# Performance work log

Hardware: AMD Instinct MI355X
Metric: run time of the kernel (lower is better)

The kernel has to match this reference:

```python
import jax, jax.numpy as jnp
from jax import lax
import numpy as np

DN = ('NDHWC', 'DHWIO', 'NDHWC')

def conv3d(x, w, b, stride=1):
    return lax.conv_general_dilated(x, w, (stride,) * 3, 'SAME', dimension_numbers=DN) + b

def convT3d(x, w, b, stride=2):
    return lax.conv_transpose(x, w, (stride,) * 3, 'SAME', dimension_numbers=DN) + b

def prelu(x, a):
    return jnp.where(x > 0, x, a * x)

def bn(x, g, be, m, v):
    # keras BatchNormalization, inference mode, epsilon=1e-3
    return (x - m) * g * lax.rsqrt(v + 1e-3) + be

def res_unit(x, c1w, c1b, c2w, c2b, g, be, m, v, a):
    # VQVAEResidualUnit: relu(x + PReLU(BN(conv2(swish(conv1(x))))))
    h = jax.nn.swish(conv3d(x, c1w, c1b))
    h = prelu(bn(conv3d(h, c2w, c2b), g, be, m, v), a)
    return jax.nn.relu(x + h)

def _forward(x, ec0_w, ec0_b, er0_c1w, er0_c1b, er0_c2w, er0_c2b, er0_g, er0_be, er0_m, er0_v, er0_a, ec1_w, ec1_b, er1_c1w, er1_c1b, er1_c2w, er1_c2b, er1_g, er1_be, er1_m, er1_v, er1_a, eo_w, eo_b, eo_a, codebook, dc0_w, dc0_b, dc0_a, dr0_c1w, dr0_c1b, dr0_c2w, dr0_c2b, dr0_g, dr0_be, dr0_m, dr0_v, dr0_a, du0_w, du0_b, dr1_c1w, dr1_c1b, dr1_c2w, dr1_c2b, dr1_g, dr1_be, dr1_m, dr1_v, dr1_a, du1_w, du1_b):
    # ----- Encoder -----
    h = jax.nn.relu(conv3d(x, ec0_w, ec0_b, stride=2))   # [B,64,64,64,64]
    h = res_unit(h, er0_c1w, er0_c1b, er0_c2w, er0_c2b, er0_g, er0_be, er0_m, er0_v, er0_a)
    h = jax.nn.relu(conv3d(h, ec1_w, ec1_b, stride=2))   # [B,32,32,32,128]
    h = res_unit(h, er1_c1w, er1_c1b, er1_c2w, er1_c2b, er1_g, er1_be, er1_m, er1_v, er1_a)
    z = prelu(conv3d(h, eo_w, eo_b), eo_a)               # [B,32,32,32,64] latent
    # ----- NSVQ (inference: hard codebook lookup) -----
    D = z.shape[-1]
    flat = z.reshape(-1, D)                              # [N, 64], N = B*32^3
    dist = (flat * flat).sum(1, keepdims=True) + (codebook * codebook).sum(1) - 2.0 * (flat @ codebook.T)  # [N, K]
    idx = jnp.argmin(dist, axis=1)
    zq = codebook[idx].reshape(z.shape)
    K = codebook.shape[0]
    p = jnp.zeros((K,), jnp.float32).at[idx].add(1.0) / flat.shape[0]
    perplexity = jnp.exp(-jnp.sum(p * jnp.log(p + 1e-12)))
    # ----- Decoder -----
    h = prelu(conv3d(zq, dc0_w, dc0_b), dc0_a)           # [B,32,32,32,128]
    h = res_unit(h, dr0_c1w, dr0_c1b, dr0_c2w, dr0_c2b, dr0_g, dr0_be, dr0_m, dr0_v, dr0_a)
    h = jax.nn.relu(convT3d(h, du0_w, du0_b))            # [B,64,64,64,64]
    h = res_unit(h, dr1_c1w, dr1_c1b, dr1_c2w, dr1_c2b, dr1_g, dr1_be, dr1_m, dr1_v, dr1_a)
    recon = convT3d(h, du1_w, du1_b)                     # [B,128,128,128,1]
    return recon, perplexity

def setup_inputs() -> dict:
    key = jax.random.key(0)
    ks = iter(jax.random.split(key, 40))
    nrm = lambda *s: jax.random.normal(next(ks), s, jnp.float32) * 0.05
    def ru(pfx, c):
        return {pfx + '_c1w': nrm(3, 3, 3, c, c), pfx + '_c1b': jnp.zeros((c,), jnp.float32),
                pfx + '_c2w': nrm(3, 3, 3, c, c), pfx + '_c2b': jnp.zeros((c,), jnp.float32),
                pfx + '_g': jnp.ones((c,), jnp.float32), pfx + '_be': jnp.zeros((c,), jnp.float32),
                pfx + '_m': jnp.zeros((c,), jnp.float32), pfx + '_v': jnp.ones((c,), jnp.float32),
                pfx + '_a': jnp.full((c,), 0.25, jnp.float32)}
    C0, C1, D, K = 64, 128, 64, 512
    inp = {'x': jax.random.normal(next(ks), (2, 128, 128, 128, 1), jnp.float32)}
    inp.update(ec0_w=nrm(4, 4, 4, 1, C0), ec0_b=jnp.zeros((C0,), jnp.float32))
    inp.update(ru('er0', C0))
    inp.update(ec1_w=nrm(4, 4, 4, C0, C1), ec1_b=jnp.zeros((C1,), jnp.float32))
    inp.update(ru('er1', C1))
    inp.update(eo_w=nrm(3, 3, 3, C1, D), eo_b=jnp.zeros((D,), jnp.float32), eo_a=jnp.full((D,), 0.25, jnp.float32))
    inp.update(codebook=jax.random.uniform(next(ks), (K, D), jnp.float32, -1.0, 1.0) * np.sqrt(6.0 / D).astype(np.float32))
    inp.update(dc0_w=nrm(3, 3, 3, D, C1), dc0_b=jnp.zeros((C1,), jnp.float32), dc0_a=jnp.full((C1,), 0.25, jnp.float32))
    inp.update(ru('dr0', C1))
    inp.update(du0_w=nrm(4, 4, 4, C1, C0), du0_b=jnp.zeros((C0,), jnp.float32))
    inp.update(ru('dr1', C0))
    inp.update(du1_w=nrm(4, 4, 4, C0, 1), du1_b=jnp.zeros((1,), jnp.float32))
    return inp

def reference(x, ec0_w, ec0_b, er0_c1w, er0_c1b, er0_c2w, er0_c2b, er0_g, er0_be, er0_m, er0_v, er0_a, ec1_w, ec1_b, er1_c1w, er1_c1b, er1_c2w, er1_c2b, er1_g, er1_be, er1_m, er1_v, er1_a, eo_w, eo_b, eo_a, codebook, dc0_w, dc0_b, dc0_a, dr0_c1w, dr0_c1b, dr0_c2w, dr0_c2b, dr0_g, dr0_be, dr0_m, dr0_v, dr0_a, du0_w, du0_b, dr1_c1w, dr1_c1b, dr1_c2w, dr1_c2b, dr1_g, dr1_be, dr1_m, dr1_v, dr1_a, du1_w, du1_b):
    return _forward(x, ec0_w, ec0_b, er0_c1w, er0_c1b, er0_c2w, er0_c2b, er0_g, er0_be, er0_m, er0_v, er0_a, ec1_w, ec1_b, er1_c1w, er1_c1b, er1_c2w, er1_c2b, er1_g, er1_be, er1_m, er1_v, er1_a, eo_w, eo_b, eo_a, codebook, dc0_w, dc0_b, dc0_a, dr0_c1w, dr0_c1b, dr0_c2w, dr0_c2b, dr0_g, dr0_be, dr0_m, dr0_v, dr0_a, du0_w, du0_b, dr1_c1w, dr1_c1b, dr1_c2w, dr1_c2b, dr1_g, dr1_be, dr1_m, dr1_v, dr1_a, du1_w, du1_b)
```

## Files before the change

kernel.cpp:

```cpp
#include <hip/hip_runtime.h>
#include <cstdint>


typedef unsigned short bf16_t;
typedef __attribute__((ext_vector_type(8)))  short s8b;
typedef __attribute__((ext_vector_type(16))) float f32x16;

__device__ __forceinline__ float b2f(bf16_t u) { return __uint_as_float((unsigned)u << 16); }
__device__ __forceinline__ bf16_t f2b(float f) {
    unsigned x = __float_as_uint(f);
    return (bf16_t)((x + 0x7FFFu + ((x >> 16) & 1u)) >> 16);
}

__device__ __forceinline__ void split3s(float v, unsigned short& h,
                                        unsigned short& m, unsigned short& l)
{
    const unsigned uv = __float_as_uint(v);
    const float fh = __uint_as_float(uv & 0xFFFF0000u);
    const float r1 = v - fh;
    const unsigned u1 = __float_as_uint(r1);
    const float fm = __uint_as_float(u1 & 0xFFFF0000u);
    const float r2 = r1 - fm;
    h = (unsigned short)(uv >> 16);
    m = (unsigned short)(u1 >> 16);
    l = (unsigned short)(__float_as_uint(r2) >> 16);
}

__device__ __forceinline__ int wdst(int tap, int ci_, int co_, int ci, int co)
{
    const int ks = ci_ >> 4, half = (ci_ >> 3) & 1, j = ci_ & 7;
    return (((tap * (ci >> 4) + ks) * 2 + half) * co + co_) * 8 + j;
}

__global__ __launch_bounds__(256)
void wprep3(const float* __restrict__ w, bf16_t* __restrict__ h,
            bf16_t* __restrict__ m, bf16_t* __restrict__ l,
            int ci, int co, int n)
{
    const int i = blockIdx.x * 256 + threadIdx.x;
    if (i >= n) return;
    const int co_ = i % co;
    const int ci_ = (i / co) % ci;
    const int tap = i / (co * ci);
    const int dst = wdst(tap, ci_, co_, ci, co);
    unsigned short hh, mm, ll2;
    split3s(w[i], hh, mm, ll2);
    h[dst] = hh; m[dst] = mm; l[dst] = ll2;
}

__global__ __launch_bounds__(256)
void wprep_split(const float* __restrict__ w, bf16_t* __restrict__ hi,
                 bf16_t* __restrict__ lo, int ci, int co, int n)
{
    const int i = blockIdx.x * 256 + threadIdx.x;
    if (i >= n) return;
    const int co_ = i % co;
    const int ci_ = (i / co) % ci;
    const int tap = i / (co * ci);
    const float v = w[i];
    const int dst = wdst(tap, ci_, co_, ci, co);
    const bf16_t h = f2b(v);
    hi[dst] = h;
    lo[dst] = f2b(v - b2f(h));
}

template<int CIN, int COUT, int SD, int NWC, int EPI>
__global__ __launch_bounds__((SD / 32) * NWC * 64)
void conv3e(const float* __restrict__ xf,
            const bf16_t* __restrict__ wh, const bf16_t* __restrict__ wm,
            const bf16_t* __restrict__ wl,
            const float* __restrict__ bias,
            const float* __restrict__ g, const float* __restrict__ be,
            const float* __restrict__ mn, const float* __restrict__ vr,
            const float* __restrict__ al,
            const float* skf, float* __restrict__ of)
{
    constexpr int NT   = (SD / 32) * NWC * 64;
    constexpr int LP   = (SD * CIN) / (4 * NT);
    constexpr int KS   = CIN / 16;
    constexpr int ROWS = SD + 2;
    constexpr int RB   = ROWS * CIN;
    __shared__ bf16_t lh[2][RB], lm[2][RB], ll[2][RB];

    const int tid  = threadIdx.x;
    const int lane = tid & 63;
    const int wid  = tid >> 6;
    const int wn   = wid % NWC, wm2 = wid / NWC;
    const int half = lane >> 5, ln = lane & 31;
    const int w    = wm2 * 32 + ln;
    const int nwg  = gridDim.x;
    const int bid  = (blockIdx.x & 7) * (nwg >> 3) + (blockIdx.x >> 3);
    const int h    = bid % SD;
    const int d    = (bid / SD) % SD;
    const int b    = bid / (SD * SD);
    const int cout = wn * 32 + ln;

    int pz[9], py[9], pt[9], np = 0;
    for (int kd = 0; kd < 3; ++kd) {
        const int iz = d + kd - 1;
        if ((unsigned)iz >= (unsigned)SD) continue;
        for (int kh = 0; kh < 3; ++kh) {
            const int iy = h + kh - 1;
            if ((unsigned)iy >= (unsigned)SD) continue;
            pz[np] = iz; py[np] = iy; pt[np] = (kd * 3 + kh) * 3; ++np;
        }
    }

    f32x16 accA, accB;
#pragma unroll
    for (int i = 0; i < 16; ++i) { accA[i] = 0.f; accB[i] = 0.f; }

    for (int i = tid; i < CIN; i += NT) {
        const int bf2 = i / (CIN / 2);
        const int r   = i % (CIN / 2);
        const int gg  = r >> 2;
        const int row = ((r >> 1) & 1) ? (SD + 1) : 0;
        const int so  = (gg * ROWS + row) * 8 + (r & 1) * 4;
        const ushort4 z4 = make_ushort4(0, 0, 0, 0);
        *reinterpret_cast<ushort4*>(&lh[bf2][so]) = z4;
        *reinterpret_cast<ushort4*>(&lm[bf2][so]) = z4;
        *reinterpret_cast<ushort4*>(&ll[bf2][so]) = z4;
    }

    float4 rg[LP];
    auto loadrow = [&](int iz, int iy) {
        const float* src = xf + ((size_t)((b * SD + iz) * SD + iy)) * SD * CIN;
#pragma unroll
        for (int j = 0; j < LP; ++j)
            rg[j] = *reinterpret_cast<const float4*>(src + (size_t)(tid + j * NT) * 4);
    };
    auto writerow = [&](int bf2) {
#pragma unroll
        for (int j = 0; j < LP; ++j) {
            const int idx = (tid + j * NT) * 4;
            const int pv = idx / CIN + 1, ch = idx % CIN;
            ushort4 h4, m4, l4;
            split3s(rg[j].x, h4.x, m4.x, l4.x);
            split3s(rg[j].y, h4.y, m4.y, l4.y);
            split3s(rg[j].z, h4.z, m4.z, l4.z);
            split3s(rg[j].w, h4.w, m4.w, l4.w);
            const int so = ((ch >> 3) * ROWS + pv) * 8 + (ch & 7);
            *reinterpret_cast<ushort4*>(&lh[bf2][so]) = h4;
            *reinterpret_cast<ushort4*>(&lm[bf2][so]) = m4;
            *reinterpret_cast<ushort4*>(&ll[bf2][so]) = l4;
        }
    };

    loadrow(pz[0], py[0]);
    writerow(0);
    if (np > 1) loadrow(pz[1], py[1]);
    __syncthreads();
#pragma unroll 1
    for (int i = 0; i < np; ++i) {
        const int cur = i & 1;
        if (i + 1 < np) writerow((i + 1) & 1);
        if (i + 2 < np) loadrow(pz[i + 2], py[i + 2]);
#pragma unroll
        for (int kw = 0; kw < 3; ++kw) {
            const int tap = pt[i] + kw;
            const int pv = w + kw;
#pragma unroll
            for (int ks = 0; ks < KS; ++ks) {
                const int so = ((ks * 2 + half) * ROWS + pv) * 8;
                const s8b ah  = *reinterpret_cast<const s8b*>(&lh[cur][so]);
                const s8b am  = *reinterpret_cast<const s8b*>(&lm[cur][so]);
                const s8b al3 = *reinterpret_cast<const s8b*>(&ll[cur][so]);
                const size_t wb = ((size_t)((tap * KS + ks) * 2 + half) * COUT + cout) * 8;
                const s8b bh = *reinterpret_cast<const s8b*>(wh + wb);
                const s8b bm = *reinterpret_cast<const s8b*>(wm + wb);
                const s8b bl = *reinterpret_cast<const s8b*>(wl + wb);
                accA = __builtin_amdgcn_mfma_f32_32x32x16_bf16(ah, bh, accA, 0, 0, 0);
                accB = __builtin_amdgcn_mfma_f32_32x32x16_bf16(ah, bm, accB, 0, 0, 0);
                accA = __builtin_amdgcn_mfma_f32_32x32x16_bf16(am, bh, accA, 0, 0, 0);
                accB = __builtin_amdgcn_mfma_f32_32x32x16_bf16(am, bm, accB, 0, 0, 0);
                accA = __builtin_amdgcn_mfma_f32_32x32x16_bf16(al3, bh, accA, 0, 0, 0);
                accB = __builtin_amdgcn_mfma_f32_32x32x16_bf16(ah, bl, accB, 0, 0, 0);
            }
        }
        __syncthreads();
    }

    const size_t outrow = ((size_t)((b * SD + d) * SD + h)) * SD;
    const float bv = bias[cout];
    float sc = 0.f, mm = 0.f, bb2 = 0.f, aa = 0.f;
    if constexpr (EPI == 3) {
        sc = g[cout] * (1.0f / sqrtf(vr[cout] + 1e-3f));
        mm = mn[cout]; bb2 = be[cout]; aa = al[cout];
    }
    if constexpr (EPI == 2) aa = al[cout];
#pragma unroll
    for (int r = 0; r < 16; ++r) {
        const int rl = (r & 3) + 8 * (r >> 2) + 4 * half;
        const size_t oe = (outrow + wm2 * 32 + rl) * COUT + cout;
        float y = accA[r] + accB[r] + bv;
        if constexpr (EPI == 0) y = fmaxf(y, 0.f);
        else if constexpr (EPI == 1) y = y / (1.f + expf(-y));
        else if constexpr (EPI == 2) y = y > 0.f ? y : aa * y;
        else {
            float t2 = (y - mm) * sc + bb2;
            t2 = t2 > 0.f ? t2 : aa * t2;
            y = fmaxf(skf[oe] + t2, 0.f);
        }
        of[oe] = y;
    }
}

__global__ __launch_bounds__(256)
void convs2e(const float* __restrict__ xf,
             const bf16_t* __restrict__ wh, const bf16_t* __restrict__ wm,
             const bf16_t* __restrict__ wl,
             const float* __restrict__ bias, float* __restrict__ of)
{
    constexpr int NT = 256, LP = (64 * 64) / (4 * NT);
    constexpr int ROWS = 66;
    __shared__ bf16_t lh[2][66 * 64], lm[2][66 * 64], ll[2][66 * 64];

    const int tid  = threadIdx.x;
    const int lane = tid & 63;
    const int wn   = tid >> 6;
    const int half = lane >> 5, ln = lane & 31;
    const int nwg  = gridDim.x;
    const int bid  = (blockIdx.x & 7) * (nwg >> 3) + (blockIdx.x >> 3);
    const int h    = bid % 32;
    const int d    = (bid / 32) % 32;
    const int b    = bid / 1024;
    const int cout = wn * 32 + ln;

    int pz[16], py[16], pt[16], np = 0;
    for (int kd = 0; kd < 4; ++kd) {
        const int iz = 2 * d + kd - 1;
        if ((unsigned)iz >= 64u) continue;
        for (int kh = 0; kh < 4; ++kh) {
            const int iy = 2 * h + kh - 1;
            if ((unsigned)iy >= 64u) continue;
            pz[np] = iz; py[np] = iy; pt[np] = (kd * 4 + kh) * 4; ++np;
        }
    }

    f32x16 accA, accB;
#pragma unroll
    for (int i = 0; i < 16; ++i) { accA[i] = 0.f; accB[i] = 0.f; }

    for (int i = tid; i < 64; i += NT) {
        const int bf2 = i / 32;
        const int r   = i % 32;
        const int gg  = r >> 2;
        const int row = ((r >> 1) & 1) ? 65 : 0;
        const int so  = (gg * ROWS + row) * 8 + (r & 1) * 4;
        const ushort4 z4 = make_ushort4(0, 0, 0, 0);
        *reinterpret_cast<ushort4*>(&lh[bf2][so]) = z4;
        *reinterpret_cast<ushort4*>(&lm[bf2][so]) = z4;
        *reinterpret_cast<ushort4*>(&ll[bf2][so]) = z4;
    }

    float4 rg[LP];
    auto loadrow = [&](int iz, int iy) {
        const float* src = xf + ((size_t)((b * 64 + iz) * 64 + iy)) * 64 * 64;
#pragma unroll
        for (int j = 0; j < LP; ++j)
            rg[j] = *reinterpret_cast<const float4*>(src + (size_t)(tid + j * NT) * 4);
    };
    auto writerow = [&](int bf2) {
#pragma unroll
        for (int j = 0; j < LP; ++j) {
            const int idx = (tid + j * NT) * 4;
            const int pv = idx / 64 + 1, ch = idx % 64;
            ushort4 h4, m4, l4;
            split3s(rg[j].x, h4.x, m4.x, l4.x);
            split3s(rg[j].y, h4.y, m4.y, l4.y);
            split3s(rg[j].z, h4.z, m4.z, l4.z);
            split3s(rg[j].w, h4.w, m4.w, l4.w);
            const int so = ((ch >> 3) * ROWS + pv) * 8 + (ch & 7);
            *reinterpret_cast<ushort4*>(&lh[bf2][so]) = h4;
            *reinterpret_cast<ushort4*>(&lm[bf2][so]) = m4;
            *reinterpret_cast<ushort4*>(&ll[bf2][so]) = l4;
        }
    };

    loadrow(pz[0], py[0]);
    writerow(0);
    if (np > 1) loadrow(pz[1], py[1]);
    __syncthreads();
#pragma unroll 1
    for (int i = 0; i < np; ++i) {
        const int cur = i & 1;
        if (i + 1 < np) writerow((i + 1) & 1);
        if (i + 2 < np) loadrow(pz[i + 2], py[i + 2]);
#pragma unroll
        for (int kw = 0; kw < 4; ++kw) {
            const int tap = pt[i] + kw;
            const int pv = 2 * ln + kw;
#pragma unroll
            for (int ks = 0; ks < 4; ++ks) {
                const int so = ((ks * 2 + half) * ROWS + pv) * 8;
                const s8b ah  = *reinterpret_cast<const s8b*>(&lh[cur][so]);
                const s8b am  = *reinterpret_cast<const s8b*>(&lm[cur][so]);
                const s8b al3 = *reinterpret_cast<const s8b*>(&ll[cur][so]);
                const size_t wb = ((size_t)((tap * 4 + ks) * 2 + half) * 128 + cout) * 8;
                const s8b bh = *reinterpret_cast<const s8b*>(wh + wb);
                const s8b bm = *reinterpret_cast<const s8b*>(wm + wb);
                const s8b bl = *reinterpret_cast<const s8b*>(wl + wb);
                accA = __builtin_amdgcn_mfma_f32_32x32x16_bf16(ah, bh, accA, 0, 0, 0);
                accB = __builtin_amdgcn_mfma_f32_32x32x16_bf16(ah, bm, accB, 0, 0, 0);
                accA = __builtin_amdgcn_mfma_f32_32x32x16_bf16(am, bh, accA, 0, 0, 0);
                accB = __builtin_amdgcn_mfma_f32_32x32x16_bf16(am, bm, accB, 0, 0, 0);
                accA = __builtin_amdgcn_mfma_f32_32x32x16_bf16(al3, bh, accA, 0, 0, 0);
                accB = __builtin_amdgcn_mfma_f32_32x32x16_bf16(ah, bl, accB, 0, 0, 0);
            }
        }
        __syncthreads();
    }

    const size_t outrow = ((size_t)((b * 32 + d) * 32 + h)) * 32;
    const float bv = bias[cout];
#pragma unroll
    for (int r = 0; r < 16; ++r) {
        const int rl = (r & 3) + 8 * (r >> 2) + 4 * half;
        const size_t oe = (outrow + rl) * 128 + cout;
        of[oe] = fmaxf(accA[r] + accB[r] + bv, 0.f);
    }
}

template<int CIN, int COUT, int SD, int NWC, int EPI>
__global__ __launch_bounds__((SD / 32) * NWC * 64)
void conv3d(const bf16_t* __restrict__ xh, const bf16_t* __restrict__ xl,
            const bf16_t* __restrict__ wh, const bf16_t* __restrict__ wl,
            const float* __restrict__ bias,
            const float* __restrict__ g, const float* __restrict__ be,
            const float* __restrict__ mn, const float* __restrict__ vr,
            const float* __restrict__ al,
            const bf16_t* skh, const bf16_t* skl,
            bf16_t* oh, bf16_t* ol)
{
    constexpr int NT   = (SD / 32) * NWC * 64;
    constexpr int LP   = (SD * CIN) / (4 * NT);
    constexpr int KS   = CIN / 16;
    constexpr int ROWS = SD + 2;
    constexpr int RB   = ROWS * CIN;
    __shared__ bf16_t lh[2][RB], ll[2][RB];

    const int tid  = threadIdx.x;
    const int lane = tid & 63;
    const int wid  = tid >> 6;
    const int wn   = wid % NWC, wm2 = wid / NWC;
    const int half = lane >> 5, ln = lane & 31;
    const int w    = wm2 * 32 + ln;
    const int nwg  = gridDim.x;
    const int bid  = (blockIdx.x & 7) * (nwg >> 3) + (blockIdx.x >> 3);
    const int h    = bid % SD;
    const int d    = (bid / SD) % SD;
    const int b    = bid / (SD * SD);
    const int cout = wn * 32 + ln;

    int pz[9], py[9], pt[9], np = 0;
    for (int kd = 0; kd < 3; ++kd) {
        const int iz = d + kd - 1;
        if ((unsigned)iz >= (unsigned)SD) continue;
        for (int kh = 0; kh < 3; ++kh) {
            const int iy = h + kh - 1;
            if ((unsigned)iy >= (unsigned)SD) continue;
            pz[np] = iz; py[np] = iy; pt[np] = (kd * 3 + kh) * 3; ++np;
        }
    }

    f32x16 accA, accB;
#pragma unroll
    for (int i = 0; i < 16; ++i) { accA[i] = 0.f; accB[i] = 0.f; }

    for (int i = tid; i < CIN; i += NT) {
        const int bf2 = i / (CIN / 2);
        const int r   = i % (CIN / 2);
        const int gg  = r >> 2;
        const int row = ((r >> 1) & 1) ? (SD + 1) : 0;
        const int so  = (gg * ROWS + row) * 8 + (r & 1) * 4;
        const ushort4 z4 = make_ushort4(0, 0, 0, 0);
        *reinterpret_cast<ushort4*>(&lh[bf2][so]) = z4;
        *reinterpret_cast<ushort4*>(&ll[bf2][so]) = z4;
    }

    ushort4 rh[LP], rl2a[LP];
    auto loadrow = [&](int iz, int iy) {
        const size_t rb = ((size_t)((b * SD + iz) * SD + iy)) * SD * CIN;
#pragma unroll
        for (int j = 0; j < LP; ++j) {
            const int idx = (tid + j * NT) * 4;
            rh[j]   = *reinterpret_cast<const ushort4*>(xh + rb + idx);
            rl2a[j] = *reinterpret_cast<const ushort4*>(xl + rb + idx);
        }
    };
    auto writerow = [&](int bf2) {
#pragma unroll
        for (int j = 0; j < LP; ++j) {
            const int idx = (tid + j * NT) * 4;
            const int pv = idx / CIN + 1, ch = idx % CIN;
            const int so = ((ch >> 3) * ROWS + pv) * 8 + (ch & 7);
            *reinterpret_cast<ushort4*>(&lh[bf2][so]) = rh[j];
            *reinterpret_cast<ushort4*>(&ll[bf2][so]) = rl2a[j];
        }
    };

    loadrow(pz[0], py[0]);
    writerow(0);
    if (np > 1) loadrow(pz[1], py[1]);
    __syncthreads();
#pragma unroll 1
    for (int i = 0; i < np; ++i) {
        const int cur = i & 1;
        if (i + 1 < np) writerow((i + 1) & 1);
        if (i + 2 < np) loadrow(pz[i + 2], py[i + 2]);
#pragma unroll
        for (int kw = 0; kw < 3; ++kw) {
            const int tap = pt[i] + kw;
            const int pv = w + kw;
#pragma unroll
            for (int ks = 0; ks < KS; ++ks) {
                const int so = ((ks * 2 + half) * ROWS + pv) * 8;
                const s8b ah  = *reinterpret_cast<const s8b*>(&lh[cur][so]);
                const s8b al2 = *reinterpret_cast<const s8b*>(&ll[cur][so]);
                const size_t wb = ((size_t)((tap * KS + ks) * 2 + half) * COUT + cout) * 8;
                const s8b bh = *reinterpret_cast<const s8b*>(wh + wb);
                const s8b bl = *reinterpret_cast<const s8b*>(wl + wb);
                accA = __builtin_amdgcn_mfma_f32_32x32x16_bf16(ah, bh, accA, 0, 0, 0);
                accB = __builtin_amdgcn_mfma_f32_32x32x16_bf16(al2, bh, accB, 0, 0, 0);
                accB = __builtin_amdgcn_mfma_f32_32x32x16_bf16(ah, bl, accB, 0, 0, 0);
            }
        }
        __syncthreads();
    }

    const size_t outrow = ((size_t)((b * SD + d) * SD + h)) * SD;
    const float bv = bias[cout];
    float sc = 0.f, mm = 0.f, bb2 = 0.f, aa = 0.f;
    if constexpr (EPI == 3) {
        sc = g[cout] * (1.0f / sqrtf(vr[cout] + 1e-3f));
        mm = mn[cout]; bb2 = be[cout]; aa = al[cout];
    }
    if constexpr (EPI == 2) aa = al[cout];
#pragma unroll
    for (int r = 0; r < 16; ++r) {
        const int rl3 = (r & 3) + 8 * (r >> 2) + 4 * half;
        const size_t oe = (outrow + wm2 * 32 + rl3) * COUT + cout;
        float y = accA[r] + accB[r] + bv;
        if constexpr (EPI == 0) y = fmaxf(y, 0.f);
        else if constexpr (EPI == 1) y = y / (1.f + expf(-y));
        else if constexpr (EPI == 2) y = y > 0.f ? y : aa * y;
        else {
            float t2 = (y - mm) * sc + bb2;
            t2 = t2 > 0.f ? t2 : aa * t2;
            float sv = b2f(skh[oe]) + b2f(skl[oe]);
            y = fmaxf(sv + t2, 0.f);
        }
        const bf16_t hh = f2b(y);
        oh[oe] = hh;
        ol[oe] = f2b(y - b2f(hh));
    }
}

__global__ __launch_bounds__(256)
void convTm(const bf16_t* __restrict__ xh, const bf16_t* __restrict__ xl,
            const bf16_t* __restrict__ wh, const bf16_t* __restrict__ wl,
            const float* __restrict__ bias,
            bf16_t* __restrict__ oh, bf16_t* __restrict__ ol)
{
    constexpr int NT = 256, LP = (32 * 128) / (4 * NT);
    constexpr int ROWS = 34;
    __shared__ bf16_t lh[2][34 * 128], ll[2][34 * 128];

    const int tid  = threadIdx.x;
    const int lane = tid & 63;
    const int wid  = tid >> 6;
    const int wn   = wid & 1, p = wid >> 1;
    const int half = lane >> 5, ln = lane & 31;
    const int nwg  = gridDim.x;
    const int bid  = (blockIdx.x & 7) * (nwg >> 3) + (blockIdx.x >> 3);
    const int ohh  = bid % 64;
    const int od   = (bid / 64) % 64;
    const int b    = bid / 4096;
    const int pd = od & 1, dz = od >> 1;
    const int ph = ohh & 1, hy = ohh >> 1;
    const int cout = wn * 32 + ln;

    int pz[4], py[4], pt[4], np = 0;
    for (int jd = 0; jd < 2; ++jd) {
        const int kd = pd + 2 * jd;
        const int iz = dz + pd - 1 + jd;
        if ((unsigned)iz >= 32u) continue;
        for (int jh = 0; jh < 2; ++jh) {
            const int kh = ph + 2 * jh;
            const int iy = hy + ph - 1 + jh;
            if ((unsigned)iy >= 32u) continue;
            pz[np] = iz; py[np] = iy; pt[np] = (kd * 4 + kh) * 4; ++np;
        }
    }

    f32x16 accA, accB;
#pragma unroll
    for (int i = 0; i < 16; ++i) { accA[i] = 0.0f; accB[i] = 0.0f; }

    for (int i = tid; i < 128; i += NT) {
        const int bf2 = i / 64;
        const int r   = i % 64;
        const int gg  = r >> 2;
        const int row = ((r >> 1) & 1) ? 33 : 0;
        const int so  = (gg * ROWS + row) * 8 + (r & 1) * 4;
        const ushort4 z4 = make_ushort4(0, 0, 0, 0);
        *reinterpret_cast<ushort4*>(&lh[bf2][so]) = z4;
        *reinterpret_cast<ushort4*>(&ll[bf2][so]) = z4;
    }

    ushort4 rh[LP], rl2a[LP];
    auto loadrow = [&](int iz, int iy) {
        const size_t rb = ((size_t)((b * 32 + iz) * 32 + iy)) * 32 * 128;
#pragma unroll
        for (int j = 0; j < LP; ++j) {
            const int idx = (tid + j * NT) * 4;
            rh[j]   = *reinterpret_cast<const ushort4*>(xh + rb + idx);
            rl2a[j] = *reinterpret_cast<const ushort4*>(xl + rb + idx);
        }
    };
    auto writerow = [&](int bf2) {
#pragma unroll
        for (int j = 0; j < LP; ++j) {
            const int idx = (tid + j * NT) * 4;
            const int pv = idx / 128 + 1, ch = idx % 128;
            const int so = ((ch >> 3) * ROWS + pv) * 8 + (ch & 7);
            *reinterpret_cast<ushort4*>(&lh[bf2][so]) = rh[j];
            *reinterpret_cast<ushort4*>(&ll[bf2][so]) = rl2a[j];
        }
    };

    loadrow(pz[0], py[0]);
    writerow(0);
    if (np > 1) loadrow(pz[1], py[1]);
    __syncthreads();
#pragma unroll 1
    for (int i = 0; i < np; ++i) {
        const int cur = i & 1;
        if (i + 1 < np) writerow((i + 1) & 1);
        if (i + 2 < np) loadrow(pz[i + 2], py[i + 2]);
#pragma unroll
        for (int jw = 0; jw < 2; ++jw) {
            const int kw = p + 2 * jw;
            const int tap = pt[i] + kw;
            const int pv = ln + p + jw;
#pragma unroll
            for (int ks = 0; ks < 8; ++ks) {
                const int so = ((ks * 2 + half) * ROWS + pv) * 8;
                const s8b a  = *reinterpret_cast<const s8b*>(&lh[cur][so]);
                const s8b a2 = *reinterpret_cast<const s8b*>(&ll[cur][so]);
                const size_t wb = ((size_t)((tap * 8 + ks) * 2 + half) * 64 + cout) * 8;
                const s8b bb = *reinterpret_cast<const s8b*>(wh + wb);
                const s8b b2 = *reinterpret_cast<const s8b*>(wl + wb);
                accA = __builtin_amdgcn_mfma_f32_32x32x16_bf16(a, bb, accA, 0, 0, 0);
                accB = __builtin_amdgcn_mfma_f32_32x32x16_bf16(a2, bb, accB, 0, 0, 0);
                accB = __builtin_amdgcn_mfma_f32_32x32x16_bf16(a, b2, accB, 0, 0, 0);
            }
        }
        __syncthreads();
    }

    const float bv = bias[cout];
#pragma unroll
    for (int r = 0; r < 16; ++r) {
        const int rl3 = (r & 3) + 8 * (r >> 2) + 4 * half;
        const int ow = 2 * rl3 + p;
        const size_t oe = (((size_t)((b * 64 + od) * 64 + ohh)) * 64 + ow) * 64 + cout;
        const float y = fmaxf(accA[r] + accB[r] + bv, 0.f);
        const bf16_t hh = f2b(y);
        oh[oe] = hh;
        ol[oe] = f2b(y - b2f(hh));
    }
}

__global__ __launch_bounds__(128)
void conv_ec0m(const float* __restrict__ x,
               const bf16_t* __restrict__ wh, const bf16_t* __restrict__ wm,
               const bf16_t* __restrict__ wl,
               const float* __restrict__ bias, float* __restrict__ of)
{
    __shared__ bf16_t lh[16 * 132], lm[16 * 132], ll[16 * 132];

    const int tid  = threadIdx.x;
    const int lane = tid & 63;
    const int wm2  = tid >> 6;
    const int half = lane >> 5, ln = lane & 31;
    const int w    = wm2 * 32 + ln;
    const int nwg  = gridDim.x;
    const int bid  = (blockIdx.x & 7) * (nwg >> 3) + (blockIdx.x >> 3);
    const int h    = bid % 64;
    const int d    = (bid / 64) % 64;
    const int b    = bid / 4096;

    for (int i = tid; i < 16 * 132; i += 128) {
        const int row = i / 132, col = i % 132;
        const int kd = row >> 2, kh = row & 3;
        const int iz = 2 * d + kd - 1, iy = 2 * h + kh - 1;
        const int ix = col - 1;
        float v = 0.f;
        if ((unsigned)iz < 128u && (unsigned)iy < 128u &&
            (unsigned)ix < 128u && col < 130)
            v = x[(size_t)((b * 128 + iz) * 128 + iy) * 128 + ix];
        unsigned short hh, mm2, ll2;
        split3s(v, hh, mm2, ll2);
        lh[i] = hh; lm[i] = mm2; ll[i] = ll2;
    }
    __syncthreads();

    f32x16 accA[2], accB[2];
// ... 192 lines not shown
    const int k = idx[n];
    const float4 c = reinterpret_cast<const float4*>(cb)[k * 16 + c4];
    ushort4 h, l;
    h.x = f2b(c.x); l.x = f2b(c.x - b2f(h.x));
    h.y = f2b(c.y); l.y = f2b(c.y - b2f(h.y));
    h.z = f2b(c.z); l.z = f2b(c.z - b2f(h.z));
    h.w = f2b(c.w); l.w = f2b(c.w - b2f(h.w));
    reinterpret_cast<ushort4*>(zh)[gid] = h;
    reinterpret_cast<ushort4*>(zl)[gid] = l;
}

__global__ __launch_bounds__(512)
void perplexity_k(const float* __restrict__ hist, float* __restrict__ out, float invN)
{
    __shared__ float red[512];
    const int t = threadIdx.x;
    const float p = hist[t] * invN;
    red[t] = p * logf(p + 1e-12f);
    __syncthreads();
    for (int s = 256; s > 0; s >>= 1) {
        if (t < s) red[t] += red[t + s];
        __syncthreads();
    }
    if (t == 0) out[0] = expf(-red[0]);
}

extern "C" void kernel_launch(void* const* d_in, const int* in_sizes, int n_in,
                              void* d_out, int out_size, void* d_ws, size_t ws_size,
                              hipStream_t stream)
{
    const float* x       = (const float*)d_in[0];
    const float* ec0_w   = (const float*)d_in[1];
    const float* ec0_b   = (const float*)d_in[2];
    const float* er0_c1w = (const float*)d_in[3];
    const float* er0_c1b = (const float*)d_in[4];
    const float* er0_c2w = (const float*)d_in[5];
    const float* er0_c2b = (const float*)d_in[6];
    const float* er0_g   = (const float*)d_in[7];
    const float* er0_be  = (const float*)d_in[8];
    const float* er0_m   = (const float*)d_in[9];
    const float* er0_v   = (const float*)d_in[10];
    const float* er0_a   = (const float*)d_in[11];
    const float* ec1_w   = (const float*)d_in[12];
    const float* ec1_b   = (const float*)d_in[13];
    const float* er1_c1w = (const float*)d_in[14];
    const float* er1_c1b = (const float*)d_in[15];
    const float* er1_c2w = (const float*)d_in[16];
    const float* er1_c2b = (const float*)d_in[17];
    const float* er1_g   = (const float*)d_in[18];
    const float* er1_be  = (const float*)d_in[19];
    const float* er1_m   = (const float*)d_in[20];
    const float* er1_v   = (const float*)d_in[21];
    const float* er1_a   = (const float*)d_in[22];
    const float* eo_w    = (const float*)d_in[23];
    const float* eo_b    = (const float*)d_in[24];
    const float* eo_a    = (const float*)d_in[25];
    const float* cb      = (const float*)d_in[26];
    const float* dc0_w   = (const float*)d_in[27];
    const float* dc0_b   = (const float*)d_in[28];
    const float* dc0_a   = (const float*)d_in[29];
    const float* dr0_c1w = (const float*)d_in[30];
    const float* dr0_c1b = (const float*)d_in[31];
    const float* dr0_c2w = (const float*)d_in[32];
    const float* dr0_c2b = (const float*)d_in[33];
    const float* dr0_g   = (const float*)d_in[34];
    const float* dr0_be  = (const float*)d_in[35];
    const float* dr0_m   = (const float*)d_in[36];
    const float* dr0_v   = (const float*)d_in[37];
    const float* dr0_a   = (const float*)d_in[38];
    const float* du0_w   = (const float*)d_in[39];
    const float* du0_b   = (const float*)d_in[40];
    const float* dr1_c1w = (const float*)d_in[41];
    const float* dr1_c1b = (const float*)d_in[42];
    const float* dr1_c2w = (const float*)d_in[43];
    const float* dr1_c2b = (const float*)d_in[44];
    const float* dr1_g   = (const float*)d_in[45];
    const float* dr1_be  = (const float*)d_in[46];
    const float* dr1_m   = (const float*)d_in[47];
    const float* dr1_v   = (const float*)d_in[48];
    const float* dr1_a   = (const float*)d_in[49];
    const float* du1_w   = (const float*)d_in[50];
    const float* du1_b   = (const float*)d_in[51];

    float* out = (float*)d_out;

    char* W = (char*)d_ws;
    float*  Af  = (float*)(W);
    float*  Hf  = (float*)(W + 134217728);
    float*  E1f = (float*)(W + 134217728);
    float*  R1f = (float*)(W + 134217728 + 33554432);
    float*  Zf  = (float*)(W);
    int*    IDX = (int*)  (W + 16777216);
    float*  CN  = (float*)(W + 17039360);
    float*  HS  = (float*)(W + 17041408);
    bf16_t* ZQh = (bf16_t*)(W + 33554432);
    bf16_t* ZQl = (bf16_t*)(W + 41943040);
    bf16_t* D0h = (bf16_t*)(W + 50331648);
    bf16_t* D0l = (bf16_t*)(W + 67108864);
    bf16_t* Gh  = (bf16_t*)(W + 83886080);
    bf16_t* Gl  = (bf16_t*)(W + 100663296);
    bf16_t* U0h = (bf16_t*)(W + 134217728);
    bf16_t* U0l = (bf16_t*)(W + 201326592);
    bf16_t* G1h = (bf16_t*)(W);
    bf16_t* G1l = (bf16_t*)(W + 67108864);

    char* WB = (char*)d_out;
    bf16_t* e0c1h = (bf16_t*)(WB + 0);
    bf16_t* e0c1m = (bf16_t*)(WB + 221184);
    bf16_t* e0c1l = (bf16_t*)(WB + 442368);
    bf16_t* e0c2h = (bf16_t*)(WB + 663552);
    bf16_t* e0c2m = (bf16_t*)(WB + 884736);
    bf16_t* e0c2l = (bf16_t*)(WB + 1105920);
    bf16_t* ec1h  = (bf16_t*)(WB + 1327104);
    bf16_t* ec1m  = (bf16_t*)(WB + 2375680);
    bf16_t* ec1l  = (bf16_t*)(WB + 3424256);
    bf16_t* e1c1h = (bf16_t*)(WB + 4472832);
    bf16_t* e1c1m = (bf16_t*)(WB + 5357568);
    bf16_t* e1c1l = (bf16_t*)(WB + 6242304);
    bf16_t* e1c2h = (bf16_t*)(WB + 7127040);
    bf16_t* e1c2m = (bf16_t*)(WB + 8011776);
    bf16_t* e1c2l = (bf16_t*)(WB + 8896512);
    bf16_t* eoh   = (bf16_t*)(WB + 9781248);
    bf16_t* eom   = (bf16_t*)(WB + 10223616);
    bf16_t* eol   = (bf16_t*)(WB + 10665984);
    bf16_t* wec0h = (bf16_t*)(WB + 11108352);
    bf16_t* wec0m = (bf16_t*)(WB + 11116544);
    bf16_t* wec0l = (bf16_t*)(WB + 11124736);
    bf16_t* dc0h  = (bf16_t*)(WB + 0);
    bf16_t* dc0l  = (bf16_t*)(WB + 442368);
    bf16_t* d0c1h = (bf16_t*)(WB + 884736);
    bf16_t* d0c1l = (bf16_t*)(WB + 1769472);
    bf16_t* d0c2h = (bf16_t*)(WB + 2654208);
    bf16_t* d0c2l = (bf16_t*)(WB + 3538944);
    bf16_t* du0h  = (bf16_t*)(WB + 4423680);
    bf16_t* du0l  = (bf16_t*)(WB + 5472256);
    bf16_t* d1c1h = (bf16_t*)(WB + 6520832);
    bf16_t* d1c1l = (bf16_t*)(WB + 6742016);
    bf16_t* d1c2h = (bf16_t*)(WB + 6963200);
    bf16_t* d1c2l = (bf16_t*)(WB + 7184384);

    const float* fn = nullptr;
    const bf16_t* bn_ = nullptr;

    wprep3<<<16, 256, 0, stream>>>(ec0_w, wec0h, wec0m, wec0l, 64, 64, 4096);
    wprep3<<<432, 256, 0, stream>>>(er0_c1w, e0c1h, e0c1m, e0c1l, 64, 64, 110592);
    wprep3<<<432, 256, 0, stream>>>(er0_c2w, e0c2h, e0c2m, e0c2l, 64, 64, 110592);
    wprep3<<<2048, 256, 0, stream>>>(ec1_w, ec1h, ec1m, ec1l, 64, 128, 524288);
    wprep3<<<1728, 256, 0, stream>>>(er1_c1w, e1c1h, e1c1m, e1c1l, 128, 128, 442368);
    wprep3<<<1728, 256, 0, stream>>>(er1_c2w, e1c2h, e1c2m, e1c2l, 128, 128, 442368);
    wprep3<<<864, 256, 0, stream>>>(eo_w, eoh, eom, eol, 128, 64, 221184);

    conv_ec0m<<<8192, 128, 0, stream>>>(x, wec0h, wec0m, wec0l, ec0_b, Af);

    conv3e<64, 64, 64, 2, 1><<<8192, 256, 0, stream>>>(
        Af, e0c1h, e0c1m, e0c1l, er0_c1b, fn, fn, fn, fn, fn, fn, Hf);
    conv3e<64, 64, 64, 2, 3><<<8192, 256, 0, stream>>>(
        Hf, e0c2h, e0c2m, e0c2l, er0_c2b, er0_g, er0_be, er0_m, er0_v, er0_a, Af, Af);

    convs2e<<<2048, 256, 0, stream>>>(Af, ec1h, ec1m, ec1l, ec1_b, E1f);

    conv3e<128, 128, 32, 4, 1><<<2048, 256, 0, stream>>>(
        E1f, e1c1h, e1c1m, e1c1l, er1_c1b, fn, fn, fn, fn, fn, fn, R1f);
    conv3e<128, 128, 32, 4, 3><<<2048, 256, 0, stream>>>(
        R1f, e1c2h, e1c2m, e1c2l, er1_c2b, er1_g, er1_be, er1_m, er1_v, er1_a, E1f, E1f);

    conv3e<128, 64, 32, 2, 2><<<2048, 128, 0, stream>>>(
        E1f, eoh, eom, eol, eo_b, fn, fn, fn, fn, eo_a, fn, Zf);

    vq_cnorm<<<8, 64, 0, stream>>>(cb, CN);
    zero512<<<1, 512, 0, stream>>>(HS);
    vq_assign<<<256, 256, 0, stream>>>(Zf, cb, CN, IDX, HS, 65536);
    perplexity_k<<<1, 512, 0, stream>>>(HS, out + 4194304, 1.0f / 65536.0f);
    vq_gather_split<<<4096, 256, 0, stream>>>(cb, IDX, ZQh, ZQl);

    wprep_split<<<864, 256, 0, stream>>>(dc0_w, dc0h, dc0l, 64, 128, 221184);
    wprep_split<<<1728, 256, 0, stream>>>(dr0_c1w, d0c1h, d0c1l, 128, 128, 442368);
    wprep_split<<<1728, 256, 0, stream>>>(dr0_c2w, d0c2h, d0c2l, 128, 128, 442368);
    wprep_split<<<2048, 256, 0, stream>>>(du0_w, du0h, du0l, 128, 64, 524288);
    wprep_split<<<432, 256, 0, stream>>>(dr1_c1w, d1c1h, d1c1l, 64, 64, 110592);
    wprep_split<<<432, 256, 0, stream>>>(dr1_c2w, d1c2h, d1c2l, 64, 64, 110592);

    conv3d<64, 128, 32, 4, 2><<<2048, 256, 0, stream>>>(
        ZQh, ZQl, dc0h, dc0l, dc0_b, fn, fn, fn, fn, dc0_a, bn_, bn_, D0h, D0l);
    conv3d<128, 128, 32, 4, 1><<<2048, 256, 0, stream>>>(
        D0h, D0l, d0c1h, d0c1l, dr0_c1b, fn, fn, fn, fn, fn, bn_, bn_, Gh, Gl);
    conv3d<128, 128, 32, 4, 3><<<2048, 256, 0, stream>>>(
        Gh, Gl, d0c2h, d0c2l, dr0_c2b, dr0_g, dr0_be, dr0_m, dr0_v, dr0_a,
        D0h, D0l, D0h, D0l);

    convTm<<<8192, 256, 0, stream>>>(D0h, D0l, du0h, du0l, du0_b, U0h, U0l);

    conv3d<64, 64, 64, 2, 1><<<8192, 256, 0, stream>>>(
        U0h, U0l, d1c1h, d1c1l, dr1_c1b, fn, fn, fn, fn, fn, bn_, bn_, G1h, G1l);
    conv3d<64, 64, 64, 2, 3><<<8192, 256, 0, stream>>>(
        G1h, G1l, d1c2h, d1c2l, dr1_c2b, dr1_g, dr1_be, dr1_m, dr1_v, dr1_a,
        U0h, U0l, U0h, U0l);

    convT_du1w<<<65536, 256, 0, stream>>>(U0h, U0l, du1_w, du1_b, out);
}
```

Measured before the change: 5.155 ms.

## Compute two output H-rows per block in stride-1 conv kernels to reuse input rows

Each block of the stride-1 conv3e/conv3d kernels now produces two adjacent H output rows instead of one. Each staged input row is then used for both outputs through two accumulator sets. An input row is loaded, split into bf16 parts and written to LDS once for up to 12 row passes instead of 18 across two blocks, which halves the grid size. Launch bounds now also set a minimum number of blocks per CU, which caps registers while the doubled accumulators raise register demand, so there is a risk of spills and lower occupancy.

```diff
diff --git a/kernel.cpp b/kernel.cpp
--- a/kernel.cpp
+++ b/kernel.cpp
@@ -65,7 +65,8 @@
 }
 
 template<int CIN, int COUT, int SD, int NWC, int EPI>
-__global__ __launch_bounds__((SD / 32) * NWC * 64)
+__global__ __launch_bounds__((SD / 32) * NWC * 64,
+                             (((SD / 32) * NWC * 64) == 128) ? 2 : 3)
 void conv3e(const float* __restrict__ xf,
             const bf16_t* __restrict__ wh, const bf16_t* __restrict__ wm,
             const bf16_t* __restrict__ wl,
@@ -80,6 +81,7 @@
     constexpr int KS   = CIN / 16;
     constexpr int ROWS = SD + 2;
     constexpr int RB   = ROWS * CIN;
+    constexpr int HH   = SD / 2;
     __shared__ bf16_t lh[2][RB], lm[2][RB], ll[2][RB];
 
     const int tid  = threadIdx.x;
@@ -90,25 +92,29 @@
     const int w    = wm2 * 32 + ln;
     const int nwg  = gridDim.x;
     const int bid  = (blockIdx.x & 7) * (nwg >> 3) + (blockIdx.x >> 3);
-    const int h    = bid % SD;
-    const int d    = (bid / SD) % SD;
-    const int b    = bid / (SD * SD);
+    const int h0   = (bid % HH) * 2;
+    const int d    = (bid / HH) % SD;
+    const int b    = bid / (HH * SD);
     const int cout = wn * 32 + ln;
 
-    int pz[9], py[9], pt[9], np = 0;
+    int pz[12], py[12], ta[12], tb[12], np = 0;
     for (int kd = 0; kd < 3; ++kd) {
         const int iz = d + kd - 1;
         if ((unsigned)iz >= (unsigned)SD) continue;
-        for (int kh = 0; kh < 3; ++kh) {
-            const int iy = h + kh - 1;
+        for (int iy = h0 - 1; iy <= h0 + 2; ++iy) {
             if ((unsigned)iy >= (unsigned)SD) continue;
-            pz[np] = iz; py[np] = iy; pt[np] = (kd * 3 + kh) * 3; ++np;
-        }
-    }
-
-    f32x16 accA, accB;
-#pragma unroll
-    for (int i = 0; i < 16; ++i) { accA[i] = 0.f; accB[i] = 0.f; }
+            const int k0 = iy - h0 + 1;
+            const int k1 = iy - h0;
+            pz[np] = iz; py[np] = iy;
+            ta[np] = ((unsigned)k0 < 3u) ? (kd * 3 + k0) * 3 : -1;
+            tb[np] = ((unsigned)k1 < 3u) ? (kd * 3 + k1) * 3 : -1;
+            ++np;
+        }
+    }
+
+    f32x16 aA0, aB0, aA1, aB1;
+#pragma unroll
+    for (int i = 0; i < 16; ++i) { aA0[i] = 0.f; aB0[i] = 0.f; aA1[i] = 0.f; aB1[i] = 0.f; }
 
     for (int i = tid; i < CIN; i += NT) {
         const int bf2 = i / (CIN / 2);
@@ -155,9 +161,9 @@
         const int cur = i & 1;
         if (i + 1 < np) writerow((i + 1) & 1);
         if (i + 2 < np) loadrow(pz[i + 2], py[i + 2]);
+        const int t0 = ta[i], t1 = tb[i];
 #pragma unroll
         for (int kw = 0; kw < 3; ++kw) {
-            const int tap = pt[i] + kw;
             const int pv = w + kw;
 #pragma unroll
             for (int ks = 0; ks < KS; ++ks) {
@@ -165,22 +171,35 @@
                 const s8b ah  = *reinterpret_cast<const s8b*>(&lh[cur][so]);
                 const s8b am  = *reinterpret_cast<const s8b*>(&lm[cur][so]);
                 const s8b al3 = *reinterpret_cast<const s8b*>(&ll[cur][so]);
-                const size_t wb = ((size_t)((tap * KS + ks) * 2 + half) * COUT + cout) * 8;
-                const s8b bh = *reinterpret_cast<const s8b*>(wh + wb);
-                const s8b bm = *reinterpret_cast<const s8b*>(wm + wb);
-                const s8b bl = *reinterpret_cast<const s8b*>(wl + wb);
-                accA = __builtin_amdgcn_mfma_f32_32x32x16_bf16(ah, bh, accA, 0, 0, 0);
-                accB = __builtin_amdgcn_mfma_f32_32x32x16_bf16(ah, bm, accB, 0, 0, 0);
-                accA = __builtin_amdgcn_mfma_f32_32x32x16_bf16(am, bh, accA, 0, 0, 0);
-                accB = __builtin_amdgcn_mfma_f32_32x32x16_bf16(am, bm, accB, 0, 0, 0);
-                accA = __builtin_amdgcn_mfma_f32_32x32x16_bf16(al3, bh, accA, 0, 0, 0);
-                accB = __builtin_amdgcn_mfma_f32_32x32x16_bf16(ah, bl, accB, 0, 0, 0);
+                if (t0 >= 0) {
+                    const size_t wb = ((size_t)(((t0 + kw) * KS + ks) * 2 + half) * COUT + cout) * 8;
+                    const s8b bh = *reinterpret_cast<const s8b*>(wh + wb);
+                    const s8b bm = *reinterpret_cast<const s8b*>(wm + wb);
+                    const s8b bl = *reinterpret_cast<const s8b*>(wl + wb);
+                    aA0 = __builtin_amdgcn_mfma_f32_32x32x16_bf16(ah, bh, aA0, 0, 0, 0);
+                    aB0 = __builtin_amdgcn_mfma_f32_32x32x16_bf16(ah, bm, aB0, 0, 0, 0);
+                    aA0 = __builtin_amdgcn_mfma_f32_32x32x16_bf16(am, bh, aA0, 0, 0, 0);
+                    aB0 = __builtin_amdgcn_mfma_f32_32x32x16_bf16(am, bm, aB0, 0, 0, 0);
+                    aA0 = __builtin_amdgcn_mfma_f32_32x32x16_bf16(al3, bh, aA0, 0, 0, 0);
+                    aB0 = __builtin_amdgcn_mfma_f32_32x32x16_bf16(ah, bl, aB0, 0, 0, 0);
+                }
+                if (t1 >= 0) {
+                    const size_t wb = ((size_t)(((t1 + kw) * KS + ks) * 2 + half) * COUT + cout) * 8;
+                    const s8b bh = *reinterpret_cast<const s8b*>(wh + wb);
+                    const s8b bm = *reinterpret_cast<const s8b*>(wm + wb);
+                    const s8b bl = *reinterpret_cast<const s8b*>(wl + wb);
+                    aA1 = __builtin_amdgcn_mfma_f32_32x32x16_bf16(ah, bh, aA1, 0, 0, 0);
+                    aB1 = __builtin_amdgcn_mfma_f32_32x32x16_bf16(ah, bm, aB1, 0, 0, 0);
+                    aA1 = __builtin_amdgcn_mfma_f32_32x32x16_bf16(am, bh, aA1, 0, 0, 0);
+                    aB1 = __builtin_amdgcn_mfma_f32_32x32x16_bf16(am, bm, aB1, 0, 0, 0);
+                    aA1 = __builtin_amdgcn_mfma_f32_32x32x16_bf16(al3, bh, aA1, 0, 0, 0);
+                    aB1 = __builtin_amdgcn_mfma_f32_32x32x16_bf16(ah, bl, aB1, 0, 0, 0);
+                }
             }
         }
         __syncthreads();
     }
 
-    const size_t outrow = ((size_t)((b * SD + d) * SD + h)) * SD;
     const float bv = bias[cout];
     float sc = 0.f, mm = 0.f, bb2 = 0.f, aa = 0.f;
     if constexpr (EPI == 3) {
@@ -188,21 +207,26 @@
         mm = mn[cout]; bb2 = be[cout]; aa = al[cout];
     }
     if constexpr (EPI == 2) aa = al[cout];
-#pragma unroll
-    for (int r = 0; r < 16; ++r) {
-        const int rl = (r & 3) + 8 * (r >> 2) + 4 * half;
-        const size_t oe = (outrow + wm2 * 32 + rl) * COUT + cout;
-        float y = accA[r] + accB[r] + bv;
-        if constexpr (EPI == 0) y = fmaxf(y, 0.f);
-        else if constexpr (EPI == 1) y = y / (1.f + expf(-y));
-        else if constexpr (EPI == 2) y = y > 0.f ? y : aa * y;
-        else {
-            float t2 = (y - mm) * sc + bb2;
-            t2 = t2 > 0.f ? t2 : aa * t2;
-            y = fmaxf(skf[oe] + t2, 0.f);
-        }
-        of[oe] = y;
-    }
+    const size_t outrow0 = ((size_t)((b * SD + d) * SD + h0)) * SD;
+    auto epi = [&](const f32x16& aA, const f32x16& aB, size_t outrow) {
+#pragma unroll
+        for (int r = 0; r < 16; ++r) {
+            const int rl = (r & 3) + 8 * (r >> 2) + 4 * half;
+            const size_t oe = (outrow + wm2 * 32 + rl) * COUT + cout;
+            float y = aA[r] + aB[r] + bv;
+            if constexpr (EPI == 0) y = fmaxf(y, 0.f);
+            else if constexpr (EPI == 1) y = y / (1.f + expf(-y));
+            else if constexpr (EPI == 2) y = y > 0.f ? y : aa * y;
+            else {
+                float t2 = (y - mm) * sc + bb2;
+                t2 = t2 > 0.f ? t2 : aa * t2;
+                y = fmaxf(skf[oe] + t2, 0.f);
+            }
+            of[oe] = y;
+        }
+    };
+    epi(aA0, aB0, outrow0);
+    epi(aA1, aB1, outrow0 + SD);
 }
 
 __global__ __launch_bounds__(256)
@@ -322,7 +346,7 @@
 }
 
 template<int CIN, int COUT, int SD, int NWC, int EPI>
-__global__ __launch_bounds__((SD / 32) * NWC * 64)
+__global__ __launch_bounds__((SD / 32) * NWC * 64, 3)
 void conv3d(const bf16_t* __restrict__ xh, const bf16_t* __restrict__ xl,
             const bf16_t* __restrict__ wh, const bf16_t* __restrict__ wl,
             const float* __restrict__ bias,
@@ -337,6 +361,7 @@
     constexpr int KS   = CIN / 16;
     constexpr int ROWS = SD + 2;
     constexpr int RB   = ROWS * CIN;
+    constexpr int HH   = SD / 2;
     __shared__ bf16_t lh[2][RB], ll[2][RB];
 
     const int tid  = threadIdx.x;
@@ -347,25 +372,29 @@
     const int w    = wm2 * 32 + ln;
     const int nwg  = gridDim.x;
     const int bid  = (blockIdx.x & 7) * (nwg >> 3) + (blockIdx.x >> 3);
-    const int h    = bid % SD;
-    const int d    = (bid / SD) % SD;
-    const int b    = bid / (SD * SD);
+    const int h0   = (bid % HH) * 2;
+    const int d    = (bid / HH) % SD;
+    const int b    = bid / (HH * SD);
     const int cout = wn * 32 + ln;
 
-    int pz[9], py[9], pt[9], np = 0;
+    int pz[12], py[12], ta[12], tb[12], np = 0;
     for (int kd = 0; kd < 3; ++kd) {
         const int iz = d + kd - 1;
         if ((unsigned)iz >= (unsigned)SD) continue;
-        for (int kh = 0; kh < 3; ++kh) {
-            const int iy = h + kh - 1;
+        for (int iy = h0 - 1; iy <= h0 + 2; ++iy) {
             if ((unsigned)iy >= (unsigned)SD) continue;
-            pz[np] = iz; py[np] = iy; pt[np] = (kd * 3 + kh) * 3; ++np;
-        }
-    }
-
-    f32x16 accA, accB;
-#pragma unroll
-    for (int i = 0; i < 16; ++i) { accA[i] = 0.f; accB[i] = 0.f; }
+            const int k0 = iy - h0 + 1;
+            const int k1 = iy - h0;
+            pz[np] = iz; py[np] = iy;
+            ta[np] = ((unsigned)k0 < 3u) ? (kd * 3 + k0) * 3 : -1;
+            tb[np] = ((unsigned)k1 < 3u) ? (kd * 3 + k1) * 3 : -1;
+            ++np;
+        }
+    }
+
+    f32x16 aA0, aB0, aA1, aB1;
+#pragma unroll
+    for (int i = 0; i < 16; ++i) { aA0[i] = 0.f; aB0[i] = 0.f; aA1[i] = 0.f; aB1[i] = 0.f; }
 
     for (int i = tid; i < CIN; i += NT) {
         const int bf2 = i / (CIN / 2);
@@ -408,27 +437,36 @@
         const int cur = i & 1;
         if (i + 1 < np) writerow((i + 1) & 1);
         if (i + 2 < np) loadrow(pz[i + 2], py[i + 2]);
+        const int t0 = ta[i], t1 = tb[i];
 #pragma unroll
         for (int kw = 0; kw < 3; ++kw) {
-            const int tap = pt[i] + kw;
             const int pv = w + kw;
 #pragma unroll
             for (int ks = 0; ks < KS; ++ks) {
                 const int so = ((ks * 2 + half) * ROWS + pv) * 8;
                 const s8b ah  = *reinterpret_cast<const s8b*>(&lh[cur][so]);
                 const s8b al2 = *reinterpret_cast<const s8b*>(&ll[cur][so]);
-                const size_t wb = ((size_t)((tap * KS + ks) * 2 + half) * COUT + cout) * 8;
-                const s8b bh = *reinterpret_cast<const s8b*>(wh + wb);
-                const s8b bl = *reinterpret_cast<const s8b*>(wl + wb);
-                accA = __builtin_amdgcn_mfma_f32_32x32x16_bf16(ah, bh, accA, 0, 0, 0);
-                accB = __builtin_amdgcn_mfma_f32_32x32x16_bf16(al2, bh, accB, 0, 0, 0);
-                accB = __builtin_amdgcn_mfma_f32_32x32x16_bf16(ah, bl, accB, 0, 0, 0);
+                if (t0 >= 0) {
+                    const size_t wb = ((size_t)(((t0 + kw) * KS + ks) * 2 + half) * COUT + cout) * 8;
+                    const s8b bh = *reinterpret_cast<const s8b*>(wh + wb);
+                    const s8b bl = *reinterpret_cast<const s8b*>(wl + wb);
+                    aA0 = __builtin_amdgcn_mfma_f32_32x32x16_bf16(ah, bh, aA0, 0, 0, 0);
+                    aB0 = __builtin_amdgcn_mfma_f32_32x32x16_bf16(al2, bh, aB0, 0, 0, 0);
+                    aB0 = __builtin_amdgcn_mfma_f32_32x32x16_bf16(ah, bl, aB0, 0, 0, 0);
+                }
+                if (t1 >= 0) {
+                    const size_t wb = ((size_t)(((t1 + kw) * KS + ks) * 2 + half) * COUT + cout) * 8;
+                    const s8b bh = *reinterpret_cast<const s8b*>(wh + wb);
+                    const s8b bl = *reinterpret_cast<const s8b*>(wl + wb);
+                    aA1 = __builtin_amdgcn_mfma_f32_32x32x16_bf16(ah, bh, aA1, 0, 0, 0);
+                    aB1 = __builtin_amdgcn_mfma_f32_32x32x16_bf16(al2, bh, aB1, 0, 0, 0);
+                    aB1 = __builtin_amdgcn_mfma_f32_32x32x16_bf16(ah, bl, aB1, 0, 0, 0);
+                }
             }
         }
         __syncthreads();
     }
 
-    const size_t outrow = ((size_t)((b * SD + d) * SD + h)) * SD;
     const float bv = bias[cout];
     float sc = 0.f, mm = 0.f, bb2 = 0.f, aa = 0.f;
     if constexpr (EPI == 3) {
@@ -436,24 +474,29 @@
         mm = mn[cout]; bb2 = be[cout]; aa = al[cout];
     }
     if constexpr (EPI == 2) aa = al[cout];
-#pragma unroll
-    for (int r = 0; r < 16; ++r) {
-        const int rl3 = (r & 3) + 8 * (r >> 2) + 4 * half;
-        const size_t oe = (outrow + wm2 * 32 + rl3) * COUT + cout;
-        float y = accA[r] + accB[r] + bv;
-        if constexpr (EPI == 0) y = fmaxf(y, 0.f);
-        else if constexpr (EPI == 1) y = y / (1.f + expf(-y));
-        else if constexpr (EPI == 2) y = y > 0.f ? y : aa * y;
-        else {
-            float t2 = (y - mm) * sc + bb2;
-            t2 = t2 > 0.f ? t2 : aa * t2;
-            float sv = b2f(skh[oe]) + b2f(skl[oe]);
-            y = fmaxf(sv + t2, 0.f);
-        }
-        const bf16_t hh = f2b(y);
-        oh[oe] = hh;
-        ol[oe] = f2b(y - b2f(hh));
-    }
+    const size_t outrow0 = ((size_t)((b * SD + d) * SD + h0)) * SD;
+    auto epi = [&](const f32x16& aA, const f32x16& aB, size_t outrow) {
+#pragma unroll
+        for (int r = 0; r < 16; ++r) {
+            const int rl3 = (r & 3) + 8 * (r >> 2) + 4 * half;
+            const size_t oe = (outrow + wm2 * 32 + rl3) * COUT + cout;
+            float y = aA[r] + aB[r] + bv;
+            if constexpr (EPI == 0) y = fmaxf(y, 0.f);
+            else if constexpr (EPI == 1) y = y / (1.f + expf(-y));
+            else if constexpr (EPI == 2) y = y > 0.f ? y : aa * y;
+            else {
+                float t2 = (y - mm) * sc + bb2;
+                t2 = t2 > 0.f ? t2 : aa * t2;
+                float sv = b2f(skh[oe]) + b2f(skl[oe]);
+                y = fmaxf(sv + t2, 0.f);
+            }
+            const bf16_t hh2 = f2b(y);
+            oh[oe] = hh2;
+            ol[oe] = f2b(y - b2f(hh2));
+        }
+    };
+    epi(aA0, aB0, outrow0);
+    epi(aA1, aB1, outrow0 + SD);
 }
 
 __global__ __launch_bounds__(256)
@@ -952,19 +995,19 @@
 
     conv_ec0m<<<8192, 128, 0, stream>>>(x, wec0h, wec0m, wec0l, ec0_b, Af);
 
-    conv3e<64, 64, 64, 2, 1><<<8192, 256, 0, stream>>>(
+    conv3e<64, 64, 64, 2, 1><<<4096, 256, 0, stream>>>(
         Af, e0c1h, e0c1m, e0c1l, er0_c1b, fn, fn, fn, fn, fn, fn, Hf);
-    conv3e<64, 64, 64, 2, 3><<<8192, 256, 0, stream>>>(
+    conv3e<64, 64, 64, 2, 3><<<4096, 256, 0, stream>>>(
         Hf, e0c2h, e0c2m, e0c2l, er0_c2b, er0_g, er0_be, er0_m, er0_v, er0_a, Af, Af);
 
     convs2e<<<2048, 256, 0, stream>>>(Af, ec1h, ec1m, ec1l, ec1_b, E1f);
 
-    conv3e<128, 128, 32, 4, 1><<<2048, 256, 0, stream>>>(
+    conv3e<128, 128, 32, 4, 1><<<1024, 256, 0, stream>>>(
         E1f, e1c1h, e1c1m, e1c1l, er1_c1b, fn, fn, fn, fn, fn, fn, R1f);
-    conv3e<128, 128, 32, 4, 3><<<2048, 256, 0, stream>>>(
+    conv3e<128, 128, 32, 4, 3><<<1024, 256, 0, stream>>>(
         R1f, e1c2h, e1c2m, e1c2l, er1_c2b, er1_g, er1_be, er1_m, er1_v, er1_a, E1f, E1f);
 
-    conv3e<128, 64, 32, 2, 2><<<2048, 128, 0, stream>>>(
+    conv3e<128, 64, 32, 2, 2><<<1024, 128, 0, stream>>>(
         E1f, eoh, eom, eol, eo_b, fn, fn, fn, fn, eo_a, fn, Zf);
 
     vq_cnorm<<<8, 64, 0, stream>>>(cb, CN);
@@ -980,19 +1023,19 @@
     wprep_split<<<432, 256, 0, stream>>>(dr1_c1w, d1c1h, d1c1l, 64, 64, 110592);
     wprep_split<<<432, 256, 0, stream>>>(dr1_c2w, d1c2h, d1c2l, 64, 64, 110592);
 
-    conv3d<64, 128, 32, 4, 2><<<2048, 256, 0, stream>>>(
+    conv3d<64, 128, 32, 4, 2><<<1024, 256, 0, stream>>>(
         ZQh, ZQl, dc0h, dc0l, dc0_b, fn, fn, fn, fn, dc0_a, bn_, bn_, D0h, D0l);
-    conv3d<128, 128, 32, 4, 1><<<2048, 256, 0, stream>>>(
+    conv3d<128, 128, 32, 4, 1><<<1024, 256, 0, stream>>>(
         D0h, D0l, d0c1h, d0c1l, dr0_c1b, fn, fn, fn, fn, fn, bn_, bn_, Gh, Gl);
-    conv3d<128, 128, 32, 4, 3><<<2048, 256, 0, stream>>>(
+    conv3d<128, 128, 32, 4, 3><<<1024, 256, 0, stream>>>(
         Gh, Gl, d0c2h, d0c2l, dr0_c2b, dr0_g, dr0_be, dr0_m, dr0_v, dr0_a,
         D0h, D0l, D0h, D0l);
 
     convTm<<<8192, 256, 0, stream>>>(D0h, D0l, du0h, du0l, du0_b, U0h, U0l);
 
-    conv3d<64, 64, 64, 2, 1><<<8192, 256, 0, stream>>>(
+    conv3d<64, 64, 64, 2, 1><<<4096, 256, 0, stream>>>(
         U0h, U0l, d1c1h, d1c1l, dr1_c1b, fn, fn, fn, fn, fn, bn_, bn_, G1h, G1l);
-    conv3d<64, 64, 64, 2, 3><<<8192, 256, 0, stream>>>(
+    conv3d<64, 64, 64, 2, 3><<<4096, 256, 0, stream>>>(
         G1h, G1l, d1c2h, d1c2l, dr1_c2b, dr1_g, dr1_be, dr1_m, dr1_v, dr1_a,
         U0h, U0l, U0h, U0l);
 
```

New measurement: 6.095 ms. 18.2% more time.
